# Performance work log

Hardware: AMD Instinct MI355X
Metric: run time of the kernel (lower is better)

Reference implementation:

```python
import jax, jax.numpy as jnp
import numpy as np

silu = jax.nn.silu
B, L, H, IN = 128, 2048, 8, 37
NL = 8  # 4 encoder + 4 decoder SE3 layers, stacked


def _se3_layer(h, pos, eW1, eb1, eW2, eb2, pW1, pb1, pW2, nW1, nb1, nW2, nb2):
    # chain graph: row = 0..N-2, col = 1..N-1 (as in the torch arange edges)
    rel = pos[1:] - pos[:-1]                      # [N-1, 3]
    dist = jnp.linalg.norm(rel, axis=-1, keepdims=True)
    ef = jnp.concatenate([h[:-1], h[1:], dist], axis=-1)   # [N-1, 2H+1]
    ea = silu(ef @ eW1 + eb1) @ eW2 + eb2                   # edge_mlp
    dp = silu(ea @ pW1 + pb1) @ pW2                         # pos_mlp (no bias on last)
    pos_upd = jnp.zeros_like(pos).at[:-1].add(dp).at[1:].add(-dp)
    node_upd = jnp.zeros_like(h).at[:-1].add(ea).at[1:].add(ea)
    h_out = silu(jnp.concatenate([h, node_upd], axis=-1) @ nW1 + nb1) @ nW2 + nb2
    return h_out, pos + 0.1 * pos_upd


def setup_inputs() -> dict:
    key = jax.random.key(0)
    ks = jax.random.split(key, 64)
    i = iter(range(64))
    def p(shape, s=0.1):
        return (jax.random.normal(ks[next(i)], shape, jnp.float32) * s)
    inp = {
        "atom_positions": jax.random.normal(ks[next(i)], (B, L, IN, 3), jnp.float32),
        "atom_mask": (jax.random.uniform(ks[next(i)], (B, L, IN)) < 0.8).astype(jnp.float32),
        "emb_W": p((IN, H)), "emb_b": p((H,)),
        "posemb_W1": p((3, H)), "posemb_b1": p((H,)),
        "posemb_W2": p((H, H)), "posemb_b2": p((H,)),
        # stacked SE3 conv params: layers 0-3 encoder, 4-7 decoder
        "conv_eW1": p((NL, 2 * H + 1, H)), "conv_eb1": p((NL, H)),
        "conv_eW2": p((NL, H, H)), "conv_eb2": p((NL, H)),
        "conv_pW1": p((NL, H, H)), "conv_pb1": p((NL, H)),
        "conv_pW2": p((NL, H, 3)),
        "conv_nW1": p((NL, 2 * H, H)), "conv_nb1": p((NL, H)),
        "conv_nW2": p((NL, H, H)), "conv_nb2": p((NL, H)),
        "tol_W1": p((H, H)), "tol_b1": p((H,)),
        "tol_W2": p((H, H)), "tol_b2": p((H,)),
        "froml_W1": p((H, H)), "froml_b1": p((H,)),
        "froml_W2": p((H, H)), "froml_b2": p((H,)),
        "posdec_W1": p((H, 2 * H)), "posdec_b1": p((2 * H,)),
        "posdec_W2": p((2 * H, IN * 3)), "posdec_b2": p((IN * 3,)),
        "maskdec_W": p((H, IN)), "maskdec_b": p((IN,)),
    }
    return inp


def reference(atom_positions, atom_mask, emb_W, emb_b, posemb_W1, posemb_b1,
              posemb_W2, posemb_b2, conv_eW1, conv_eb1, conv_eW2, conv_eb2,
              conv_pW1, conv_pb1, conv_pW2, conv_nW1, conv_nb1, conv_nW2,
              conv_nb2, tol_W1, tol_b1, tol_W2, tol_b2, froml_W1, froml_b1,
              froml_W2, froml_b2, posdec_W1, posdec_b1, posdec_W2, posdec_b2,
              maskdec_W, maskdec_b):
    # ---- encode ----
    h = atom_mask @ emb_W + emb_b                              # [B,L,H]
    m = atom_mask[..., None]
    mean_pos = (atom_positions * m).sum(axis=2) / (m.sum(axis=2) + 1e-8)  # [B,L,3]
    pos_feat = silu(mean_pos @ posemb_W1 + posemb_b1) @ posemb_W2 + posemb_b2
    h = (h + pos_feat).reshape(B * L, H)
    pos = mean_pos.reshape(B * L, 3)
    for li in range(4):
        h, pos = _se3_layer(h, pos, conv_eW1[li], conv_eb1[li], conv_eW2[li],
                            conv_eb2[li], conv_pW1[li], conv_pb1[li], conv_pW2[li],
                            conv_nW1[li], conv_nb1[li], conv_nW2[li], conv_nb2[li])
    h = h.reshape(B, L, H)
    z = silu(h @ tol_W1 + tol_b1) @ tol_W2 + tol_b2            # [B,L,latent]
    # ---- decode ----
    h = silu(z @ froml_W1 + froml_b1) @ froml_W2 + froml_b2
    h = h.reshape(B * L, H)
    pos = pos  # already flat [B*L, 3]
    for li in range(4, 8):
        h, pos = _se3_layer(h, pos, conv_eW1[li], conv_eb1[li], conv_eW2[li],
                            conv_eb2[li], conv_pW1[li], conv_pb1[li], conv_pW2[li],
                            conv_nW1[li], conv_nb1[li], conv_nW2[li], conv_nb2[li])
    h = h.reshape(B, L, H)
    pos_out = (silu(h @ posdec_W1 + posdec_b1) @ posdec_W2 + posdec_b2)
    pos_out = pos_out.reshape(B, L, IN, 3)
    mask_out = h @ maskdec_W + maskdec_b                       # [B,L,IN]
    return pos_out, mask_out
```

## Files before the change

kernel.cpp:

```cpp
#include <hip/hip_runtime.h>

#define NTOT 262144
#define NLAY 8
#define TOUT 240

__device__ __forceinline__ float silu_f(float x) {
    return x * (1.0f / (1.0f + __expf(-x)));
}

__global__ __launch_bounds__(256) void k_encode(
    const float* __restrict__ ap, const float* __restrict__ amask,
    const float* __restrict__ embW, const float* __restrict__ embB,
    const float* __restrict__ peW1, const float* __restrict__ peB1,
    const float* __restrict__ peW2, const float* __restrict__ peB2,
    float* __restrict__ h0, float* __restrict__ pos0)
{
    __shared__ alignas(16) float sM[64 * 37];
    __shared__ alignas(16) float sA[64 * 111];
    const int tid = threadIdx.x;
    const long nb = (long)blockIdx.x * 64;

    const float4* gm = (const float4*)(amask + nb * 37);
    float4* sm4 = (float4*)sM;
    #pragma unroll 1
    for (int i = tid; i < 64 * 37 / 4; i += 256) sm4[i] = gm[i];
    const float4* ga = (const float4*)(ap + nb * 111);
    float4* sa4 = (float4*)sA;
    #pragma unroll 1
    for (int i = tid; i < 64 * 111 / 4; i += 256) sa4[i] = ga[i];
    __syncthreads();

    if (tid < 64) {
        const float* mrow = sM + tid * 37;
        const float* arow = sA + tid * 111;
        float hacc[8];
        #pragma unroll
        for (int j = 0; j < 8; ++j) hacc[j] = embB[j];
        float ps0 = 0.f, ps1 = 0.f, ps2 = 0.f, msum = 0.f;
        #pragma unroll 1
        for (int k = 0; k < 37; ++k) {
            float mv = mrow[k];
            msum += mv;
            #pragma unroll
            for (int j = 0; j < 8; ++j) hacc[j] += mv * embW[k * 8 + j];
            ps0 += mv * arow[k * 3 + 0];
            ps1 += mv * arow[k * 3 + 1];
            ps2 += mv * arow[k * 3 + 2];
        }
        float inv = 1.0f / (msum + 1e-8f);
        float mp0 = ps0 * inv, mp1 = ps1 * inv, mp2 = ps2 * inv;
        float q[8];
        #pragma unroll
        for (int j = 0; j < 8; ++j) {
            float a = peB1[j];
            a += mp0 * peW1[0 * 8 + j];
            a += mp1 * peW1[1 * 8 + j];
            a += mp2 * peW1[2 * 8 + j];
            q[j] = silu_f(a);
        }
        #pragma unroll
        for (int j = 0; j < 8; ++j) {
            float a = peB2[j];
            #pragma unroll
            for (int r = 0; r < 8; ++r) a += q[r] * peW2[r * 8 + j];
            hacc[j] += a;
        }
        const long g = nb + tid;
        float4* hd = (float4*)(h0 + g * 8);
        hd[0] = make_float4(hacc[0], hacc[1], hacc[2], hacc[3]);
        hd[1] = make_float4(hacc[4], hacc[5], hacc[6], hacc[7]);
        ((float4*)pos0)[g] = make_float4(mp0, mp1, mp2, 0.f);
    }
}

__global__ __launch_bounds__(256) void k_stack(
    const float* __restrict__ h0, const float* __restrict__ pos0,
    float* __restrict__ hfin,
    const float* __restrict__ ceW1, const float* __restrict__ ceB1,
    const float* __restrict__ ceW2, const float* __restrict__ ceB2,
    const float* __restrict__ cpW1, const float* __restrict__ cpB1,
    const float* __restrict__ cpW2,
    const float* __restrict__ cnW1, const float* __restrict__ cnB1,
    const float* __restrict__ cnW2, const float* __restrict__ cnB2,
    const float* __restrict__ tW1, const float* __restrict__ tB1,
    const float* __restrict__ tW2, const float* __restrict__ tB2,
    const float* __restrict__ fW1, const float* __restrict__ fB1,
    const float* __restrict__ fW2, const float* __restrict__ fB2)
{
    __shared__ float4 sH[512];
    __shared__ float4 sP[256];
    __shared__ float4 sE[512];
    __shared__ float4 sD[256];
    const int t = threadIdx.x;
    const int g0 = blockIdx.x * TOUT;
    const int g = g0 - 8 + t;

    float4 z4 = make_float4(0.f, 0.f, 0.f, 0.f);
    float4 ha = z4, hb = z4, pa = z4;
    if (g >= 0 && g < NTOT) {
        const float4* hp = (const float4*)(h0 + (long)g * 8);
        ha = hp[0];
        hb = hp[1];
        pa = ((const float4*)pos0)[g];
    }
    sH[t * 2] = ha;
    sH[t * 2 + 1] = hb;
    sP[t] = pa;
    __syncthreads();

    const int tp = (t < 255) ? (t + 1) : t;
    const int tm = (t > 0) ? (t - 1) : t;
    float hn[8] = {0, 0, 0, 0, 0, 0, 0, 0};

    #pragma unroll 1
    for (int li = 0; li < NLAY; ++li) {
        float hl[8], hr[8];
        {
            float4 a = sH[t * 2], b = sH[t * 2 + 1];
            hl[0] = a.x; hl[1] = a.y; hl[2] = a.z; hl[3] = a.w;
            hl[4] = b.x; hl[5] = b.y; hl[6] = b.z; hl[7] = b.w;
            float4 c = sH[tp * 2], d = sH[tp * 2 + 1];
            hr[0] = c.x; hr[1] = c.y; hr[2] = c.z; hr[3] = c.w;
            hr[4] = d.x; hr[5] = d.y; hr[6] = d.z; hr[7] = d.w;
        }
        float4 plv = sP[t], prv = sP[tp];
        float r0 = prv.x - plv.x, r1 = prv.y - plv.y, r2 = prv.z - plv.z;
        float dist = sqrtf(r0 * r0 + r1 * r1 + r2 * r2);

        const float* wE1 = ceW1 + li * 136;
        const float* bE1 = ceB1 + li * 8;
        const float* wE2 = ceW2 + li * 64;
        const float* bE2 = ceB2 + li * 8;
        const float* wP1 = cpW1 + li * 64;
        const float* bP1 = cpB1 + li * 8;
        const float* wP2 = cpW2 + li * 24;
        const float* wN1 = cnW1 + li * 128;
        const float* bN1 = cnB1 + li * 8;
        const float* wN2 = cnW2 + li * 64;
        const float* bN2 = cnB2 + li * 8;

        float t1[8];
        #pragma unroll
        for (int j = 0; j < 8; ++j) {
            float a = bE1[j];
            #pragma unroll
            for (int r = 0; r < 8; ++r) a += hl[r] * wE1[r * 8 + j];
            #pragma unroll
            for (int r = 0; r < 8; ++r) a += hr[r] * wE1[64 + r * 8 + j];
            a += dist * wE1[128 + j];
            t1[j] = silu_f(a);
        }
        float ea[8];
        #pragma unroll
        for (int j = 0; j < 8; ++j) {
            float a = bE2[j];
            #pragma unroll
            for (int r = 0; r < 8; ++r) a += t1[r] * wE2[r * 8 + j];
            ea[j] = a;
        }
        float q[8];
        #pragma unroll
        for (int j = 0; j < 8; ++j) {
            float a = bP1[j];
            #pragma unroll
            for (int r = 0; r < 8; ++r) a += ea[r] * wP1[r * 8 + j];
            q[j] = silu_f(a);
        }
        float dp0 = 0.f, dp1 = 0.f, dp2 = 0.f;
        #pragma unroll
        for (int r = 0; r < 8; ++r) {
            dp0 += q[r] * wP2[r * 3 + 0];
            dp1 += q[r] * wP2[r * 3 + 1];
            dp2 += q[r] * wP2[r * 3 + 2];
        }
        sE[t * 2] = make_float4(ea[0], ea[1], ea[2], ea[3]);
        sE[t * 2 + 1] = make_float4(ea[4], ea[5], ea[6], ea[7]);
        sD[t] = make_float4(dp0, dp1, dp2, 0.f);
        __syncthreads();

        float nu[8] = {0, 0, 0, 0, 0, 0, 0, 0};
        float pu0 = 0.f, pu1 = 0.f, pu2 = 0.f;
        if (g < NTOT - 1) {
            #pragma unroll
            for (int j = 0; j < 8; ++j) nu[j] += ea[j];
            pu0 += dp0; pu1 += dp1; pu2 += dp2;
        }
        if (g > 0) {
            float4 a = sE[tm * 2], b = sE[tm * 2 + 1];
            nu[0] += a.x; nu[1] += a.y; nu[2] += a.z; nu[3] += a.w;
            nu[4] += b.x; nu[5] += b.y; nu[6] += b.z; nu[7] += b.w;
            float4 dl = sD[tm];
            pu0 -= dl.x; pu1 -= dl.y; pu2 -= dl.z;
        }
        float u[8];
        #pragma unroll
        for (int j = 0; j < 8; ++j) {
            float a = bN1[j];
            #pragma unroll
            for (int r = 0; r < 8; ++r) a += hl[r] * wN1[r * 8 + j];
            #pragma unroll
            for (int r = 0; r < 8; ++r) a += nu[r] * wN1[64 + r * 8 + j];
            u[j] = silu_f(a);
        }
        #pragma unroll
        for (int j = 0; j < 8; ++j) {
            float a = bN2[j];
            #pragma unroll
            for (int r = 0; r < 8; ++r) a += u[r] * wN2[r * 8 + j];
            hn[j] = a;
        }
        float pn0 = plv.x + 0.1f * pu0;
        float pn1 = plv.y + 0.1f * pu1;
        float pn2 = plv.z + 0.1f * pu2;

        if (li == 3) {
            float a8[8];
            #pragma unroll
            for (int j = 0; j < 8; ++j) {
                float a = tB1[j];
                #pragma unroll
                for (int r = 0; r < 8; ++r) a += hn[r] * tW1[r * 8 + j];
                a8[j] = silu_f(a);
            }
            float zz[8];
            #pragma unroll
            for (int j = 0; j < 8; ++j) {
                float a = tB2[j];
                #pragma unroll
                for (int r = 0; r < 8; ++r) a += a8[r] * tW2[r * 8 + j];
                zz[j] = a;
            }
            float b8[8];
            #pragma unroll
            for (int j = 0; j < 8; ++j) {
                float a = fB1[j];
                #pragma unroll
                for (int r = 0; r < 8; ++r) a += zz[r] * fW1[r * 8 + j];
                b8[j] = silu_f(a);
            }
            #pragma unroll
            for (int j = 0; j < 8; ++j) {
                float a = fB2[j];
                #pragma unroll
                for (int r = 0; r < 8; ++r) a += b8[r] * fW2[r * 8 + j];
                hn[j] = a;
            }
        }

        const int winLo2 = max(0, g0 - 7 + li);
        const int winHi2 = min(NTOT, g0 + 247 - li);
        if (g >= winLo2 && g < winHi2) {
            sH[t * 2] = make_float4(hn[0], hn[1], hn[2], hn[3]);
            sH[t * 2 + 1] = make_float4(hn[4], hn[5], hn[6], hn[7]);
            sP[t] = make_float4(pn0, pn1, pn2, 0.f);
        }
        __syncthreads();
    }

    if (t >= 8 && t < 8 + TOUT && g < NTOT) {
        float4* hd = (float4*)(hfin + (long)g * 8);
        hd[0] = make_float4(hn[0], hn[1], hn[2], hn[3]);
        hd[1] = make_float4(hn[4], hn[5], hn[6], hn[7]);
    }
}

__global__ __launch_bounds__(256) void k_decode(
    const float* __restrict__ hfin,
    const float* __restrict__ dW1, const float* __restrict__ dB1,
    const float* __restrict__ dW2, const float* __restrict__ dB2,
    const float* __restrict__ mW, const float* __restrict__ mB,
    float* __restrict__ out)
{
    __shared__ alignas(16) float sh[128 * 8];
    __shared__ float st1[128 * 16];
    const int tid = threadIdx.x;
    const long nb = (long)blockIdx.x * 128;

    ((float4*)sh)[tid] = ((const float4*)(hfin + nb * 8))[tid];
    __syncthreads();

    {
        const int n = tid >> 1;
        const int c0 = (tid & 1) * 8;
        const float* hr = sh + n * 8;
        #pragma unroll
        for (int jj = 0; jj < 8; ++jj) {
            int j = c0 + jj;
            float a = dB1[j];
            #pragma unroll
            for (int r = 0; r < 8; ++r) a += hr[r] * dW1[r * 16 + j];
            st1[n * 16 + j] = silu_f(a);
        }
    }
    __syncthreads();

    const long posBase = nb * 111;
    #pragma unroll 1
    for (int o = tid; o < 128 * 111; o += 256) {
        unsigned n = (unsigned)o / 111u;
        unsigned j = (unsigned)o - n * 111u;
        float a = dB2[j];
        const float* t1r = st1 + n * 16;
        #pragma unroll
        for (int r = 0; r < 16; ++r) a += t1r[r] * dW2[r * 111 + j];
        out[posBase + o] = a;
    }
    const long mBase = (long)NTOT * 111 + nb * 37;
    #pragma unroll 1
    for (int o = tid; o < 128 * 37; o += 256) {
        unsigned n = (unsigned)o / 37u;
        unsigned j = (unsigned)o - n * 37u;
        float a = mB[j];
        const float* hr = sh + n * 8;
        #pragma unroll
        for (int r = 0; r < 8; ++r) a += hr[r] * mW[r * 37 + j];
        out[mBase + o] = a;
    }
}

extern "C" void kernel_launch(void* const* d_in, const int* in_sizes, int n_in,
                              void* d_out, int out_size, void* d_ws, size_t ws_size,
                              hipStream_t stream) {
    const float* ap     = (const float*)d_in[0];
    const float* amask  = (const float*)d_in[1];
    const float* embW   = (const float*)d_in[2];
    const float* embB   = (const float*)d_in[3];
    const float* peW1   = (const float*)d_in[4];
    const float* peB1   = (const float*)d_in[5];
    const float* peW2   = (const float*)d_in[6];
    const float* peB2   = (const float*)d_in[7];
    const float* ceW1   = (const float*)d_in[8];
    const float* ceB1   = (const float*)d_in[9];
    const float* ceW2   = (const float*)d_in[10];
    const float* ceB2   = (const float*)d_in[11];
    const float* cpW1   = (const float*)d_in[12];
    const float* cpB1   = (const float*)d_in[13];
    const float* cpW2   = (const float*)d_in[14];
    const float* cnW1   = (const float*)d_in[15];
    const float* cnB1   = (const float*)d_in[16];
    const float* cnW2   = (const float*)d_in[17];
    const float* cnB2   = (const float*)d_in[18];
    const float* tW1    = (const float*)d_in[19];
    const float* tB1    = (const float*)d_in[20];
    const float* tW2    = (const float*)d_in[21];
    const float* tB2    = (const float*)d_in[22];
    const float* fW1    = (const float*)d_in[23];
    const float* fB1    = (const float*)d_in[24];
    const float* fW2    = (const float*)d_in[25];
    const float* fB2    = (const float*)d_in[26];
    const float* dW1    = (const float*)d_in[27];
    const float* dB1    = (const float*)d_in[28];
    const float* dW2    = (const float*)d_in[29];
    const float* dB2    = (const float*)d_in[30];
    const float* mW     = (const float*)d_in[31];
    const float* mB     = (const float*)d_in[32];

    float* h0   = (float*)d_ws;
    float* pos0 = h0 + (size_t)NTOT * 8;
    float* hfin = pos0 + (size_t)NTOT * 4;
    float* out  = (float*)d_out;

    k_encode<<<NTOT / 64, 256, 0, stream>>>(ap, amask, embW, embB,
                                            peW1, peB1, peW2, peB2, h0, pos0);
    k_stack<<<(NTOT + TOUT - 1) / TOUT, 256, 0, stream>>>(
        h0, pos0, hfin,
        ceW1, ceB1, ceW2, ceB2, cpW1, cpB1, cpW2,
        cnW1, cnB1, cnW2, cnB2,
        tW1, tB1, tW2, tB2, fW1, fB1, fW2, fB2);
    k_decode<<<NTOT / 128, 256, 0, stream>>>(hfin, dW1, dB1, dW2, dB2, mW, mB, out);
}
```

Measured before the change: 521.8 us.

## Parallelize encode over four lanes per node and restructure decode output loops

```diff
diff --git a/kernel.cpp b/kernel.cpp
--- a/kernel.cpp
+++ b/kernel.cpp
@@ -17,9 +17,11 @@
 {
     __shared__ alignas(16) float sM[64 * 37];
     __shared__ alignas(16) float sA[64 * 111];
+    __shared__ alignas(16) float sW[37 * 8];
     const int tid = threadIdx.x;
     const long nb = (long)blockIdx.x * 64;
 
+    if (tid < 74) ((float4*)sW)[tid] = ((const float4*)embW)[tid];
     const float4* gm = (const float4*)(amask + nb * 37);
     float4* sm4 = (float4*)sM;
     #pragma unroll 1
@@ -30,47 +32,61 @@
     for (int i = tid; i < 64 * 111 / 4; i += 256) sa4[i] = ga[i];
     __syncthreads();
 
-    if (tid < 64) {
-        const float* mrow = sM + tid * 37;
-        const float* arow = sA + tid * 111;
-        float hacc[8];
-        #pragma unroll
-        for (int j = 0; j < 8; ++j) hacc[j] = embB[j];
-        float ps0 = 0.f, ps1 = 0.f, ps2 = 0.f, msum = 0.f;
-        #pragma unroll 1
-        for (int k = 0; k < 37; ++k) {
-            float mv = mrow[k];
-            msum += mv;
-            #pragma unroll
-            for (int j = 0; j < 8; ++j) hacc[j] += mv * embW[k * 8 + j];
-            ps0 += mv * arow[k * 3 + 0];
-            ps1 += mv * arow[k * 3 + 1];
-            ps2 += mv * arow[k * 3 + 2];
-        }
-        float inv = 1.0f / (msum + 1e-8f);
-        float mp0 = ps0 * inv, mp1 = ps1 * inv, mp2 = ps2 * inv;
-        float q[8];
-        #pragma unroll
-        for (int j = 0; j < 8; ++j) {
-            float a = peB1[j];
-            a += mp0 * peW1[0 * 8 + j];
-            a += mp1 * peW1[1 * 8 + j];
-            a += mp2 * peW1[2 * 8 + j];
-            q[j] = silu_f(a);
-        }
-        #pragma unroll
-        for (int j = 0; j < 8; ++j) {
-            float a = peB2[j];
-            #pragma unroll
-            for (int r = 0; r < 8; ++r) a += q[r] * peW2[r * 8 + j];
-            hacc[j] += a;
-        }
-        const long g = nb + tid;
-        float4* hd = (float4*)(h0 + g * 8);
-        hd[0] = make_float4(hacc[0], hacc[1], hacc[2], hacc[3]);
-        hd[1] = make_float4(hacc[4], hacc[5], hacc[6], hacc[7]);
-        ((float4*)pos0)[g] = make_float4(mp0, mp1, mp2, 0.f);
-    }
+    const int n = tid >> 2;
+    const int p = tid & 3;
+    const int k0 = p * 10;
+    const int k1 = (p == 3) ? 37 : k0 + 10;
+
+    const float* mrow = sM + n * 37;
+    const float* arow = sA + n * 111;
+    float hacc[8] = {0, 0, 0, 0, 0, 0, 0, 0};
+    float ps0 = 0.f, ps1 = 0.f, ps2 = 0.f, msum = 0.f;
+    #pragma unroll 1
+    for (int k = k0; k < k1; ++k) {
+        float mv = mrow[k];
+        msum += mv;
+        const float4* wr = (const float4*)(sW + k * 8);
+        float4 w0 = wr[0], w1 = wr[1];
+        hacc[0] += mv * w0.x; hacc[1] += mv * w0.y;
+        hacc[2] += mv * w0.z; hacc[3] += mv * w0.w;
+        hacc[4] += mv * w1.x; hacc[5] += mv * w1.y;
+        hacc[6] += mv * w1.z; hacc[7] += mv * w1.w;
+        ps0 += mv * arow[k * 3 + 0];
+        ps1 += mv * arow[k * 3 + 1];
+        ps2 += mv * arow[k * 3 + 2];
+    }
+    #pragma unroll
+    for (int m = 1; m <= 2; m <<= 1) {
+        msum += __shfl_xor(msum, m);
+        ps0 += __shfl_xor(ps0, m);
+        ps1 += __shfl_xor(ps1, m);
+        ps2 += __shfl_xor(ps2, m);
+        #pragma unroll
+        for (int j = 0; j < 8; ++j) hacc[j] += __shfl_xor(hacc[j], m);
+    }
+
+    float inv = 1.0f / (msum + 1e-8f);
+    float mp0 = ps0 * inv, mp1 = ps1 * inv, mp2 = ps2 * inv;
+    float q[8];
+    #pragma unroll
+    for (int j = 0; j < 8; ++j) {
+        float a = peB1[j];
+        a += mp0 * peW1[0 * 8 + j];
+        a += mp1 * peW1[1 * 8 + j];
+        a += mp2 * peW1[2 * 8 + j];
+        q[j] = silu_f(a);
+    }
+    #pragma unroll
+    for (int j = 0; j < 8; ++j) {
+        float a = peB2[j] + embB[j];
+        #pragma unroll
+        for (int r = 0; r < 8; ++r) a += q[r] * peW2[r * 8 + j];
+        hacc[j] += a;
+    }
+    const long g = nb + n;
+    if (p == 0) ((float4*)(h0 + g * 8))[0] = make_float4(hacc[0], hacc[1], hacc[2], hacc[3]);
+    if (p == 1) ((float4*)(h0 + g * 8))[1] = make_float4(hacc[4], hacc[5], hacc[6], hacc[7]);
+    if (p == 2) ((float4*)pos0)[g] = make_float4(mp0, mp1, mp2, 0.f);
 }
 
 __global__ __launch_bounds__(256) void k_stack(
@@ -272,7 +288,7 @@
     float* __restrict__ out)
 {
     __shared__ alignas(16) float sh[128 * 8];
-    __shared__ float st1[128 * 16];
+    __shared__ alignas(16) float st1[128 * 16];
     const int tid = threadIdx.x;
     const long nb = (long)blockIdx.x * 128;
 
@@ -282,7 +298,9 @@
     {
         const int n = tid >> 1;
         const int c0 = (tid & 1) * 8;
-        const float* hr = sh + n * 8;
+        const float4* h4 = (const float4*)(sh + n * 8);
+        float4 h0v = h4[0], h1v = h4[1];
+        float hr[8] = {h0v.x, h0v.y, h0v.z, h0v.w, h1v.x, h1v.y, h1v.z, h1v.w};
         #pragma unroll
         for (int jj = 0; jj < 8; ++jj) {
             int j = c0 + jj;
@@ -294,27 +312,41 @@
     }
     __syncthreads();
 
-    const long posBase = nb * 111;
-    #pragma unroll 1
-    for (int o = tid; o < 128 * 111; o += 256) {
-        unsigned n = (unsigned)o / 111u;
-        unsigned j = (unsigned)o - n * 111u;
-        float a = dB2[j];
-        const float* t1r = st1 + n * 16;
-        #pragma unroll
-        for (int r = 0; r < 16; ++r) a += t1r[r] * dW2[r * 111 + j];
-        out[posBase + o] = a;
-    }
-    const long mBase = (long)NTOT * 111 + nb * 37;
-    #pragma unroll 1
-    for (int o = tid; o < 128 * 37; o += 256) {
-        unsigned n = (unsigned)o / 37u;
-        unsigned j = (unsigned)o - n * 37u;
-        float a = mB[j];
-        const float* hr = sh + n * 8;
-        #pragma unroll
-        for (int r = 0; r < 8; ++r) a += hr[r] * mW[r * 37 + j];
-        out[mBase + o] = a;
+    if (tid < 222) {
+        const int half = (tid >= 111) ? 1 : 0;
+        const int j = tid - half * 111;
+        float w[16];
+        #pragma unroll
+        for (int r = 0; r < 16; ++r) w[r] = dW2[r * 111 + j];
+        const float bj = dB2[j];
+        float* op = out + nb * 111 + j;
+        #pragma unroll 2
+        for (int n = half; n < 128; n += 2) {
+            const float4* t4 = (const float4*)(st1 + n * 16);
+            float4 a0 = t4[0], a1 = t4[1], a2 = t4[2], a3 = t4[3];
+            float acc = bj;
+            acc += a0.x * w[0] + a0.y * w[1] + a0.z * w[2] + a0.w * w[3];
+            acc += a1.x * w[4] + a1.y * w[5] + a1.z * w[6] + a1.w * w[7];
+            acc += a2.x * w[8] + a2.y * w[9] + a2.z * w[10] + a2.w * w[11];
+            acc += a3.x * w[12] + a3.y * w[13] + a3.z * w[14] + a3.w * w[15];
+            op[n * 111] = acc;
+        }
+        const int g6 = tid / 37;
+        const int j2 = tid - g6 * 37;
+        float wm[8];
+        #pragma unroll
+        for (int r = 0; r < 8; ++r) wm[r] = mW[r * 37 + j2];
+        const float bm = mB[j2];
+        float* omp_ = out + (long)NTOT * 111 + nb * 37 + j2;
+        #pragma unroll 1
+        for (int n = g6; n < 128; n += 6) {
+            const float4* h4 = (const float4*)(sh + n * 8);
+            float4 h0v = h4[0], h1v = h4[1];
+            float acc = bm;
+            acc += h0v.x * wm[0] + h0v.y * wm[1] + h0v.z * wm[2] + h0v.w * wm[3];
+            acc += h1v.x * wm[4] + h1v.y * wm[5] + h1v.z * wm[6] + h1v.w * wm[7];
+            omp_[n * 37] = acc;
+        }
     }
 }
 
```

Measured after the change: 433.7 us. 16.9% less time.
